# Optimization experiments

Measured on AMD Instinct MI355X. Metric: run time of the kernel, lower is better.

The kernel has to match this reference:

```python
import jax, jax.numpy as jnp
import numpy as np

N = 50000          # total nodes
B = 10             # graphs in batch
NPG = N // B       # nodes per graph (equal-sized graphs)
E = 800000         # edges
IN_DIM = 128
HID = 128
NHEAD = 4
DHEAD = HID // NHEAD
T = 1000
SLOPE = 0.2        # leaky_relu negative slope
ALPHA_L = 2.0


def _ln(x, g=None, b=None, eps=1e-5):
    mu = jnp.mean(x, axis=-1, keepdims=True)
    var = jnp.var(x, axis=-1, keepdims=True)
    y = (x - mu) * jax.lax.rsqrt(var + eps)
    if g is not None:
        y = y * g + b
    return y


def _gatv2(h, src, dst, Ws, Wd, a, b):
    # DGL GATv2Conv, share_weights=False, residual=False, bias=True, activation=gelu
    fs = (h @ Ws).reshape(N, NHEAD, DHEAD)
    fd = (h @ Wd).reshape(N, NHEAD, DHEAD)
    # per-edge attention logits [E, NHEAD]
    e = jnp.sum(jax.nn.leaky_relu(fs[src] + fd[dst], SLOPE) * a, axis=-1)
    # edge softmax grouped by destination node
    m = jax.ops.segment_max(e, dst, num_segments=N)
    ee = jnp.exp(e - m[dst])
    den = jax.ops.segment_sum(ee, dst, num_segments=N)
    alpha = ee / den[dst]                                  # [E, NHEAD]
    rst = jax.ops.segment_sum(alpha[..., None] * fs[src], dst, num_segments=N)
    rst = jax.nn.gelu(rst + b.reshape(1, NHEAD, DHEAD), approximate=False)
    return rst.reshape(N, HID)


def _forward(x, noise, sab, somab, time_emb,
             Ws0, Wd0, a0, b0, g0, be0,
             Ws1, Wd1, a1, b1, g1, be1,
             Wo1, bo1, Wo2, bo2, src, dst, t):
    # sample_q: statistics-matched signed noise
    miu = jnp.mean(x, axis=0)
    std = jnp.std(x, axis=0, ddof=1)          # torch.std is unbiased
    nz = _ln(noise) * std + miu
    nz = jnp.sign(x) * jnp.abs(nz)
    s1 = jnp.repeat(sab[t], NPG)[:, None]
    s2 = jnp.repeat(somab[t], NPG)[:, None]
    x_t = s1 * x + s2 * nz
    temb = jnp.repeat(time_emb[t], NPG, axis=0)
    # Denoising_Unet
    h = jnp.concatenate([x_t, temb], axis=1)   # [N, IN_DIM+HID]
    h = _ln(_gatv2(h, src, dst, Ws0, Wd0, a0, b0), g0, be0)
    h_in = h
    h = _gatv2(h, src, dst, Ws1, Wd1, a1, b1)
    h = _ln(h + h_in, g1, be1)                 # residual (shapes match)
    out = jax.nn.relu(h @ Wo1 + bo1) @ Wo2 + bo2
    # loss_fn
    mse = jnp.mean((out - x) ** 2)
    on = out / jnp.maximum(jnp.linalg.norm(out, axis=-1, keepdims=True), 1e-12)
    xn = x / jnp.maximum(jnp.linalg.norm(x, axis=-1, keepdims=True), 1e-12)
    cos = jnp.mean((1.0 - jnp.sum(on * xn, axis=-1)) ** ALPHA_L)
    return mse + 0.1 * cos


def setup_inputs() -> dict:
    key = jax.random.key(0)
    ks = jax.random.split(key, 26)
    betas = np.linspace(1e-4, 0.02, T, dtype=np.float64)
    ab = np.cumprod(1.0 - betas)
    s = 0.02
    in0 = IN_DIM + HID
    inp = {}
    inp['x'] = jax.random.normal(ks[0], (N, IN_DIM), jnp.float32)
    inp['noise'] = jax.random.normal(ks[1], (N, IN_DIM), jnp.float32)
    inp['src'] = jax.random.randint(ks[2], (E,), 0, N, dtype=jnp.int32)
    inp['dst'] = jax.random.randint(ks[3], (E,), 0, N, dtype=jnp.int32)
    inp['t'] = jax.random.randint(ks[4], (B,), 0, T, dtype=jnp.int32)
    inp['sab'] = jnp.asarray(np.sqrt(ab), jnp.float32)
    inp['somab'] = jnp.asarray(np.sqrt(1.0 - ab), jnp.float32)
    inp['time_emb'] = jax.random.normal(ks[5], (T, HID), jnp.float32) * s
    inp['Ws0'] = jax.random.normal(ks[6], (in0, HID), jnp.float32) * s
    inp['Wd0'] = jax.random.normal(ks[7], (in0, HID), jnp.float32) * s
    inp['a0'] = jax.random.normal(ks[8], (NHEAD, DHEAD), jnp.float32) * s
    inp['b0'] = jnp.zeros((HID,), jnp.float32)
    inp['g0'] = jnp.ones((HID,), jnp.float32)
    inp['be0'] = jnp.zeros((HID,), jnp.float32)
    inp['Ws1'] = jax.random.normal(ks[9], (HID, HID), jnp.float32) * s
    inp['Wd1'] = jax.random.normal(ks[10], (HID, HID), jnp.float32) * s
    inp['a1'] = jax.random.normal(ks[11], (NHEAD, DHEAD), jnp.float32) * s
    inp['b1'] = jnp.zeros((HID,), jnp.float32)
    inp['g1'] = jnp.ones((HID,), jnp.float32)
    inp['be1'] = jnp.zeros((HID,), jnp.float32)
    inp['Wo1'] = jax.random.normal(ks[12], (HID, HID), jnp.float32) * s
    inp['bo1'] = jnp.zeros((HID,), jnp.float32)
    inp['Wo2'] = jax.random.normal(ks[13], (HID, IN_DIM), jnp.float32) * s
    inp['bo2'] = jnp.zeros((IN_DIM,), jnp.float32)
    return inp


def reference(x, noise, src, dst, t, sab, somab, time_emb,
              Ws0, Wd0, a0, b0, g0, be0,
              Ws1, Wd1, a1, b1, g1, be1,
              Wo1, bo1, Wo2, bo2):
    return _forward(x, noise, sab, somab, time_emb,
                    Ws0, Wd0, a0, b0, g0, be0,
                    Ws1, Wd1, a1, b1, g1, be1,
                    Wo1, bo1, Wo2, bo2, src, dst, t)
```

## Files before the change

kernel.cpp:

```cpp
#include <hip/hip_runtime.h>
#include <hip/hip_bf16.h>
#include <math.h>

#define NN 50000
#define EE 800000
#define NPG 5000

typedef short bf16x8 __attribute__((ext_vector_type(8)));
typedef float f32x4 __attribute__((ext_vector_type(4)));

__device__ __forceinline__ float gelu_exact(float v) {
    return 0.5f * v * (1.0f + erff(v * 0.70710678118654752440f));
}

__device__ __forceinline__ ushort f2b(float f) {
    union { float f; uint u; } v; v.f = f;
    uint r = (v.u + 0x7fffu + ((v.u >> 16) & 1)) >> 16;
    return (ushort)r;
}
__device__ __forceinline__ uint pack2(float a, float b) {
    return (uint)f2b(a) | ((uint)f2b(b) << 16);
}
__device__ __forceinline__ float blo(uint u) {
    union { uint u; float f; } v; v.u = u << 16; return v.f;
}
__device__ __forceinline__ float bhi(uint u) {
    union { uint u; float f; } v; v.u = u & 0xffff0000u; return v.f;
}

__global__ __launch_bounds__(256) void head1_kernel(const float* __restrict__ x,
        float* __restrict__ sums, const int* __restrict__ dst, int* __restrict__ counts,
        const float* __restrict__ Ws0, const float* __restrict__ Wd0,
        const float* __restrict__ Ws1, const float* __restrict__ Wd1,
        const float* __restrict__ Wo1, const float* __restrict__ Wo2,
        ushort* __restrict__ Wt0, ushort* __restrict__ Wt1,
        ushort* __restrict__ Wo1t, ushort* __restrict__ Wo2t) {
    int bid = blockIdx.x;
    int tid = threadIdx.x;
    if (bid < 1024) {
        int col4 = (tid & 31) * 4;
        int rowgrp = tid >> 5;
        float s0 = 0.f, s1 = 0.f, s2 = 0.f, s3 = 0.f;
        float q0 = 0.f, q1 = 0.f, q2 = 0.f, q3 = 0.f;
        for (int r = bid * 8 + rowgrp; r < NN; r += 8192) {
            float4 v = *(const float4*)(x + (size_t)r * 128 + col4);
            s0 += v.x; s1 += v.y; s2 += v.z; s3 += v.w;
            q0 += v.x * v.x; q1 += v.y * v.y; q2 += v.z * v.z; q3 += v.w * v.w;
        }
        s0 += __shfl_xor(s0, 32); s1 += __shfl_xor(s1, 32);
        s2 += __shfl_xor(s2, 32); s3 += __shfl_xor(s3, 32);
        q0 += __shfl_xor(q0, 32); q1 += __shfl_xor(q1, 32);
        q2 += __shfl_xor(q2, 32); q3 += __shfl_xor(q3, 32);
        __shared__ float red[4][32][8];
        int wv = tid >> 6, l = tid & 63;
        if (l < 32) {
            float* p = red[wv][l];
            p[0] = s0; p[1] = s1; p[2] = s2; p[3] = s3;
            p[4] = q0; p[5] = q1; p[6] = q2; p[7] = q3;
        }
        __syncthreads();
        if (tid < 32) {
            float a0 = 0.f, a1 = 0.f, a2 = 0.f, a3 = 0.f;
            float b0 = 0.f, b1 = 0.f, b2 = 0.f, b3 = 0.f;
#pragma unroll
            for (int w = 0; w < 4; ++w) {
                float* p = red[w][tid];
                a0 += p[0]; a1 += p[1]; a2 += p[2]; a3 += p[3];
                b0 += p[4]; b1 += p[5]; b2 += p[6]; b3 += p[7];
            }
            int c = tid * 4;
            atomicAdd(&sums[c], a0); atomicAdd(&sums[c + 1], a1);
            atomicAdd(&sums[c + 2], a2); atomicAdd(&sums[c + 3], a3);
            atomicAdd(&sums[128 + c], b0); atomicAdd(&sums[128 + c + 1], b1);
            atomicAdd(&sums[128 + c + 2], b2); atomicAdd(&sums[128 + c + 3], b3);
        }
    } else if (bid < 4149) {
        int i = (bid - 1024) * 256 + tid;
        if (i < EE) atomicAdd(&counts[dst[i]], 1);
    } else {
        int i = (bid - 4149) * 256 + tid;
        if (i < 65536) {
            int c = i >> 8, k = i & 255;
            const float* W = (c < 128) ? Ws0 : Wd0;
            Wt0[c * 256 + k] = f2b(W[k * 128 + (c & 127)]);
        } else if (i < 98304) {
            int j = i - 65536;
            int c = j >> 7, k = j & 127;
            const float* W = (c < 128) ? Ws1 : Wd1;
            Wt1[c * 128 + k] = f2b(W[k * 128 + (c & 127)]);
        } else if (i < 114688) {
            int j = i - 98304;
            int c = j >> 7, k = j & 127;
            Wo1t[c * 128 + k] = f2b(Wo1[k * 128 + c]);
        } else if (i < 131072) {
            int j = i - 114688;
            int c = j >> 7, k = j & 127;
            Wo2t[c * 128 + k] = f2b(Wo2[k * 128 + c]);
        }
    }
}

__global__ __launch_bounds__(1024) void head2_kernel(const int* __restrict__ counts,
        int* __restrict__ blockSums, float* __restrict__ stats, int n) {
    int bid = blockIdx.x;
    int tid = threadIdx.x;
    if (bid < 49) {
        int i = bid * 1024 + tid;
        int v = (i < n) ? counts[i] : 0;
#pragma unroll
        for (int o = 32; o > 0; o >>= 1) v += __shfl_down(v, o);
        __shared__ int sh[16];
        int lane = tid & 63, wv = tid >> 6;
        if (lane == 0) sh[wv] = v;
        __syncthreads();
        if (tid == 0) {
            int s = 0;
#pragma unroll
            for (int k = 0; k < 16; ++k) s += sh[k];
            blockSums[bid] = s;
        }
    } else {
        if (tid < 128) {
            int c = tid;
            float sum = stats[c], sumsq = stats[128 + c];
            float mu = sum / (float)n;
            float var = (sumsq - sum * sum / (float)n) / (float)(n - 1);
            stats[256 + c] = mu;
            stats[384 + c] = sqrtf(fmaxf(var, 0.f));
        }
    }
}

__global__ __launch_bounds__(1024) void head3_kernel(const float* __restrict__ x,
        const float* __restrict__ noise, const int* __restrict__ t,
        const float* __restrict__ sab, const float* __restrict__ somab,
        const float* __restrict__ temb, const float* __restrict__ stats,
        ushort* __restrict__ h,
        const int* __restrict__ counts, const int* __restrict__ blockSums,
        int* __restrict__ indptr, int* __restrict__ cursor, int n) {
    int bid = blockIdx.x;
    int tid = threadIdx.x;
    if (bid < 3125) {
        int wid = bid * 16 + (tid >> 6);
        int lane = tid & 63;
        int tt = t[wid / NPG];
        float s1 = sab[tt], s2v = somab[tt];
        float2 nz = ((const float2*)noise)[(size_t)wid * 64 + lane];
        float s = nz.x + nz.y;
        float sq = nz.x * nz.x + nz.y * nz.y;
#pragma unroll
        for (int o = 1; o < 64; o <<= 1) { s += __shfl_xor(s, o); sq += __shfl_xor(sq, o); }
        float mu = s * (1.f / 128.f);
        float var = sq * (1.f / 128.f) - mu * mu;
        float r = rsqrtf(var + 1e-5f);
        int f0 = 2 * lane, f1 = f0 + 1;
        float y0 = (nz.x - mu) * r * stats[384 + f0] + stats[256 + f0];
        float y1 = (nz.y - mu) * r * stats[384 + f1] + stats[256 + f1];
        float2 xv = ((const float2*)x)[(size_t)wid * 64 + lane];
        float sg0 = (xv.x > 0.f) ? 1.f : ((xv.x < 0.f) ? -1.f : 0.f);
        float sg1 = (xv.y > 0.f) ? 1.f : ((xv.y < 0.f) ? -1.f : 0.f);
        float n0 = sg0 * fabsf(y0);
        float n1 = sg1 * fabsf(y1);
        float xt0 = s1 * xv.x + s2v * n0;
        float xt1 = s1 * xv.y + s2v * n1;
        uint* row = (uint*)(h + (size_t)wid * 256);
        row[lane] = pack2(xt0, xt1);
        float2 te = ((const float2*)(temb + (size_t)tt * 128))[lane];
        row[64 + lane] = pack2(te.x, te.y);
    } else {
        int b = bid - 3125;
        __shared__ int sOff, sTot;
        if (tid < 64) {
            int v = (tid < 49) ? blockSums[tid] : 0;
            int incl = v;
#pragma unroll
            for (int o = 1; o < 64; o <<= 1) {
                int tv = __shfl_up(incl, o);
                if ((tid & 63) >= o) incl += tv;
            }
            int off = (b == 0) ? 0 : __shfl(incl, b - 1);
            int tot = __shfl(incl, 48);
            if (tid == 0) { sOff = off; sTot = tot; }
        }
        __syncthreads();
        int i = b * 1024 + tid;
        int v = (i < n) ? counts[i] : 0;
        int lane = tid & 63, wv = tid >> 6;
        int incl = v;
#pragma unroll
        for (int o = 1; o < 64; o <<= 1) {
            int tv = __shfl_up(incl, o);
            if (lane >= o) incl += tv;
        }
        __shared__ int wsum[16];
        __shared__ int woff[16];
        if (lane == 63) wsum[wv] = incl;
        __syncthreads();
        if (tid == 0) {
            int s = 0;
#pragma unroll
            for (int k = 0; k < 16; ++k) { woff[k] = s; s += wsum[k]; }
        }
        __syncthreads();
        int ex = incl - v + woff[wv] + sOff;
        if (i < n) { indptr[i] = ex; cursor[i] = ex; }
        if (b == 48 && tid == 0) indptr[n] = sTot;
    }
}

__global__ __launch_bounds__(1024) void scatter_kernel(const int* __restrict__ src,
        const int* __restrict__ dst, int* __restrict__ cursor,
        int* __restrict__ csr_src, int e) {
    int i = blockIdx.x * 1024 + threadIdx.x;
    if (i < e) {
        int p = atomicAdd(&cursor[dst[i]], 1);
        csr_src[p] = src[i];
    }
}

template<int K, int NCOL, int EPI>
__global__ __launch_bounds__(256, 2) void mfma_gemm(const ushort* __restrict__ A,
        const ushort* __restrict__ Wt, const float* __restrict__ bias,
        ushort* __restrict__ C0, ushort* __restrict__ C1,
        float* __restrict__ Cf, int M) {
    constexpr int NFRAG = NCOL / 16;
    constexpr int KSTEPS = K / 32;
    __shared__ ushort Bs[32 * NCOL];
    int tid = threadIdx.x;
    int wave = tid >> 6, lane = tid & 63;
    int l15 = lane & 15, g = lane >> 4;
    int rowBase = blockIdx.x * 64 + wave * 16;
    int r = rowBase + l15;
    int rc = min(r, M - 1);
    const ushort* Arow = A + (size_t)rc * K + g * 8;

    f32x4 acc[NFRAG] = {};

    for (int ks = 0; ks < KSTEPS; ++ks) {
#pragma unroll
        for (int i = 0; i < NCOL / 64; ++i) {
            int ch = tid + i * 256;
            int c = ch >> 2, q = ch & 3;
            float4 v = *(const float4*)(Wt + (size_t)c * K + ks * 32 + q * 8);
            int off = c * 64 + ((q * 16) ^ ((c & 7) << 4));
            *(float4*)((char*)Bs + off) = v;
        }
        __syncthreads();
        bf16x8 af = *(const bf16x8*)(Arow + ks * 32);
        int roff = l15 * 64 + ((g * 16) ^ ((l15 & 7) << 4));
#pragma unroll
        for (int n = 0; n < NFRAG; ++n) {
            bf16x8 bf = *(const bf16x8*)((const char*)Bs + n * 1024 + roff);
            acc[n] = __builtin_amdgcn_mfma_f32_16x16x32_bf16(af, bf, acc[n], 0, 0, 0);
        }
        __syncthreads();
    }

#pragma unroll
    for (int n = 0; n < NFRAG; ++n) {
        int col = n * 16 + l15;
#pragma unroll
        for (int j = 0; j < 4; ++j) {
            int row = rowBase + g * 4 + j;
            if (row < M) {
                float v = acc[n][j];
                if (EPI == 1) v = fmaxf(v + bias[col], 0.f);
                if (EPI == 2) v = v + bias[col];
                if (EPI == 2) {
                    Cf[(size_t)row * 128 + col] = v;
                } else {
                    ushort bv = f2b(v);
                    if (NCOL == 256) {
                        if (n < 8) C0[(size_t)row * 128 + col] = bv;
                        else       C1[(size_t)row * 128 + col - 128] = bv;
                    } else {
                        C0[(size_t)row * 128 + col] = bv;
                    }
                }
            }
        }
    }
}

__global__ __launch_bounds__(256) void gat_ln_kernel(const ushort* __restrict__ fs,
        const ushort* __restrict__ fd, const float* __restrict__ a,
        const float* __restrict__ bias, const int* __restrict__ indptr,
        const int* __restrict__ csr_src, const float* __restrict__ resid,
        const float* __restrict__ g, const float* __restrict__ be,
        float* __restrict__ outF, ushort* __restrict__ outB, int n) {
    int wid = (blockIdx.x * blockDim.x + threadIdx.x) >> 6;
    int lane = threadIdx.x & 63;
    if (wid >= n) return;
    int beg = indptr[wid], cnt = indptr[wid + 1] - beg;
    const int* ip = csr_src + beg;
    uint fdu = ((const uint*)fd)[(size_t)wid * 64 + lane];
    float fd0 = blo(fdu), fd1 = bhi(fdu);
    float a0 = a[2 * lane], a1 = a[2 * lane + 1];
    const uint* fsu = (const uint*)fs;

    int e0 = (0 < cnt) ? ip[0] : 0;
    int e1 = (1 < cnt) ? ip[1] : 0;
    int e2 = (2 < cnt) ? ip[2] : 0;
    int e3 = (3 < cnt) ? ip[3] : 0;
    int e4 = (4 < cnt) ? ip[4] : 0;
    int e5 = (5 < cnt) ? ip[5] : 0;
    int e6 = (6 < cnt) ? ip[6] : 0;
    int e7 = (7 < cnt) ? ip[7] : 0;
    uint v0 = fsu[(size_t)e0 * 64 + lane];
    uint v1 = fsu[(size_t)e1 * 64 + lane];
    uint v2 = fsu[(size_t)e2 * 64 + lane];
    uint v3 = fsu[(size_t)e3 * 64 + lane];
    uint v4 = fsu[(size_t)e4 * 64 + lane];
    uint v5 = fsu[(size_t)e5 * 64 + lane];
    uint v6 = fsu[(size_t)e6 * 64 + lane];
    uint v7 = fsu[(size_t)e7 * 64 + lane];

    float den = 0.f, acc0 = 0.f, acc1 = 0.f;
    for (int j = 0; j < cnt; ++j) {
        uint cur = v0;
        v0 = v1; v1 = v2; v2 = v3; v3 = v4; v4 = v5; v5 = v6; v6 = v7;
        int nj = j + 8;
        int ni = (nj < cnt) ? ip[nj] : 0;
        v7 = fsu[(size_t)ni * 64 + lane];
        float c0f = blo(cur), c1f = bhi(cur);
        float t0 = c0f + fd0; t0 = (t0 > 0.f ? t0 : 0.2f * t0) * a0;
        float t1 = c1f + fd1; t1 = (t1 > 0.f ? t1 : 0.2f * t1) * a1;
        float p = t0 + t1;
        p += __shfl_xor(p, 1); p += __shfl_xor(p, 2);
        p += __shfl_xor(p, 4); p += __shfl_xor(p, 8);
        float w = __expf(p);
        den += w;
        acc0 = fmaf(w, c0f, acc0);
        acc1 = fmaf(w, c1f, acc1);
    }

    float inv = (cnt > 0) ? 1.f / den : 0.f;
    float r0 = gelu_exact(acc0 * inv + bias[2 * lane]);
    float r1 = gelu_exact(acc1 * inv + bias[2 * lane + 1]);
    if (resid) {
        float2 rr = ((const float2*)resid)[(size_t)wid * 64 + lane];
        r0 += rr.x; r1 += rr.y;
    }
    float s = r0 + r1;
    float sq = r0 * r0 + r1 * r1;
#pragma unroll
    for (int o = 1; o < 64; o <<= 1) { s += __shfl_xor(s, o); sq += __shfl_xor(sq, o); }
    float mu = s * (1.f / 128.f);
    float var = sq * (1.f / 128.f) - mu * mu;
    float rstd = rsqrtf(var + 1e-5f);
    float2 gg = ((const float2*)g)[lane];
    float2 bb = ((const float2*)be)[lane];
    float o0 = (r0 - mu) * rstd * gg.x + bb.x;
    float o1 = (r1 - mu) * rstd * gg.y + bb.y;
    if (outF) ((float2*)outF)[(size_t)wid * 64 + lane] = make_float2(o0, o1);
    if (outB) ((uint*)outB)[(size_t)wid * 64 + lane] = pack2(o0, o1);
}

__global__ __launch_bounds__(256) void loss_partial_kernel(const float* __restrict__ out,
        const float* __restrict__ x, float* __restrict__ partials, int n) {
    __shared__ float sm[8];
    int lane = threadIdx.x & 63;
    int wv = threadIdx.x >> 6;
    int gw = blockIdx.x * 4 + wv;
    float d2 = 0.f, closs = 0.f;
    for (int row = gw; row < n; row += 4096) {
        float2 o = ((const float2*)out)[(size_t)row * 64 + lane];
        float2 xv = ((const float2*)x)[(size_t)row * 64 + lane];
        float e0 = o.x - xv.x, e1 = o.y - xv.y;
        d2 += e0 * e0 + e1 * e1;
        float oo = o.x * o.x + o.y * o.y;
        float xx = xv.x * xv.x + xv.y * xv.y;
        float ox = o.x * xv.x + o.y * xv.y;
#pragma unroll
        for (int s = 1; s < 64; s <<= 1) {
            oo += __shfl_xor(oo, s); xx += __shfl_xor(xx, s); ox += __shfl_xor(ox, s);
        }
        float no = fmaxf(sqrtf(oo), 1e-12f);
        float nx = fmaxf(sqrtf(xx), 1e-12f);
        float cs = 1.f - ox / (no * nx);
        closs += cs * cs;
    }
#pragma unroll
    for (int s = 1; s < 64; s <<= 1) d2 += __shfl_xor(d2, s);
    if (lane == 0) { sm[wv] = d2; sm[4 + wv] = closs; }
    __syncthreads();
    if (threadIdx.x == 0) {
        partials[2 * blockIdx.x] = sm[0] + sm[1] + sm[2] + sm[3];
        partials[2 * blockIdx.x + 1] = sm[4] + sm[5] + sm[6] + sm[7];
    }
}

__global__ __launch_bounds__(1024) void loss_final_kernel(const float* __restrict__ partials,
        float* __restrict__ outp, int nb, int n) {
    __shared__ double sd[32];
    int tid = threadIdx.x;
    double m = 0.0, c = 0.0;
    for (int i = tid; i < nb; i += 1024) { m += partials[2 * i]; c += partials[2 * i + 1]; }
#pragma unroll
    for (int s = 1; s < 64; s <<= 1) { m += __shfl_xor(m, s); c += __shfl_xor(c, s); }
    int wv = tid >> 6, lane = tid & 63;
    if (lane == 0) { sd[wv] = m; sd[16 + wv] = c; }
    __syncthreads();
    if (tid == 0) {
        double mt = 0.0, ct = 0.0;
        for (int i = 0; i < 16; ++i) { mt += sd[i]; ct += sd[16 + i]; }
        outp[0] = (float)(mt / ((double)n * 128.0) + 0.1 * ct / (double)n);
    }
}

extern "C" void kernel_launch(void* const* d_in, const int* in_sizes, int n_in,
                              void* d_out, int out_size, void* d_ws, size_t ws_size,
                              hipStream_t stream) {
    const int N = NN, E = EE;
    const float* x     = (const float*)d_in[0];
    const float* noise = (const float*)d_in[1];
    const int*   src   = (const int*)d_in[2];
    const int*   dst   = (const int*)d_in[3];
    const int*   t     = (const int*)d_in[4];
    const float* sab   = (const float*)d_in[5];
    const float* somab = (const float*)d_in[6];
    const float* temb  = (const float*)d_in[7];
    const float* Ws0   = (const float*)d_in[8];
    const float* Wd0   = (const float*)d_in[9];
    const float* a0    = (const float*)d_in[10];
    const float* b0    = (const float*)d_in[11];
    const float* g0    = (const float*)d_in[12];
    const float* be0   = (const float*)d_in[13];
    const float* Ws1   = (const float*)d_in[14];
    const float* Wd1   = (const float*)d_in[15];
    const float* a1    = (const float*)d_in[16];
    const float* b1    = (const float*)d_in[17];
    const float* g1    = (const float*)d_in[18];
    const float* be1   = (const float*)d_in[19];
    const float* Wo1   = (const float*)d_in[20];
    const float* bo1   = (const float*)d_in[21];
    const float* Wo2   = (const float*)d_in[22];
    const float* bo2   = (const float*)d_in[23];

    float* ws = (float*)d_ws;
    ushort* hB  = (ushort*)ws;
    ushort* Pb  = (ushort*)ws;
    ushort* fsB = (ushort*)(ws + (size_t)N * 128);
    ushort* fdB = (ushort*)(ws + (size_t)N * 192);
    float*  P   = ws + (size_t)N * 256;
    float*  outb = P;
    ushort* Qb  = fdB;
    ushort* z   = fsB;
    float* wtail = ws + (size_t)N * 384;
    ushort* Wt0  = (ushort*)wtail;
    ushort* Wt1  = (ushort*)(wtail + 32768);
    ushort* Wo1t = (ushort*)(wtail + 49152);
    ushort* Wo2t = (ushort*)(wtail + 57344);
    float* stats    = wtail + 65536;
    float* partials = stats + 512;
    int* counts  = (int*)(partials + 2048);
    int* indptr  = counts + N;
    int* cursor  = indptr + N + 1;
    int* csr_src = cursor + N;
    int* blockSums = csr_src + E;

    hipMemsetAsync(stats, 0, 512 * sizeof(float), stream);
    hipMemsetAsync(counts, 0, (size_t)N * sizeof(int), stream);

    head1_kernel<<<4661, 256, 0, stream>>>(x, stats, dst, counts,
                                           Ws0, Wd0, Ws1, Wd1, Wo1, Wo2,
                                           Wt0, Wt1, Wo1t, Wo2t);
    head2_kernel<<<50, 1024, 0, stream>>>(counts, blockSums, stats, N);
    head3_kernel<<<3174, 1024, 0, stream>>>(x, noise, t, sab, somab, temb, stats, hB,
                                            counts, blockSums, indptr, cursor, N);
    scatter_kernel<<<(E + 1023) / 1024, 1024, 0, stream>>>(src, dst, cursor, csr_src, E);

    int gemmGrid = (N + 63) / 64;
    mfma_gemm<256, 256, 0><<<gemmGrid, 256, 0, stream>>>(hB, Wt0, nullptr, fsB, fdB, nullptr, N);
    gat_ln_kernel<<<(N + 3) / 4, 256, 0, stream>>>(fsB, fdB, a0, b0, indptr, csr_src,
                                                   nullptr, g0, be0, P, Pb, N);
    mfma_gemm<128, 256, 0><<<gemmGrid, 256, 0, stream>>>(Pb, Wt1, nullptr, fsB, fdB, nullptr, N);
    gat_ln_kernel<<<(N + 3) / 4, 256, 0, stream>>>(fsB, fdB, a1, b1, indptr, csr_src,
                                                   P, g1, be1, nullptr, Qb, N);
    mfma_gemm<128, 128, 1><<<gemmGrid, 256, 0, stream>>>(Qb, Wo1t, bo1, z, nullptr, nullptr, N);
    mfma_gemm<128, 128, 2><<<gemmGrid, 256, 0, stream>>>(z, Wo2t, bo2, nullptr, nullptr, outb, N);

    loss_partial_kernel<<<1024, 256, 0, stream>>>(outb, x, partials, N);
    loss_final_kernel<<<1, 1024, 0, stream>>>(partials, (float*)d_out, 1024, N);
}
```

Measured before the change: 454.8 us.

## Fuse loss into final GEMM epilogue and vectorize GAT aggregation per quad

The final output GEMM now computes the MSE and cosine loss terms in its epilogue and accumulates them with atomics. This removes the fp32 output buffer write, the separate loss_partial pass and the multi-block final reduction. The GAT kernel now handles four edges at once, one per 16-lane quad, with each lane loading 16 bytes (8 bf16), which cuts serial loop iterations and shuffle depth. The layer-1 residual is also read from the bf16 copy instead of a separate fp32 copy, which drops that fp32 write and trades some precision and ordering determinism of the float atomics for lower memory traffic.

```diff
diff --git a/kernel.cpp b/kernel.cpp
--- a/kernel.cpp
+++ b/kernel.cpp
@@ -26,6 +26,10 @@
 }
 __device__ __forceinline__ float bhi(uint u) {
     union { uint u; float f; } v; v.u = u & 0xffff0000u; return v.f;
+}
+__device__ __forceinline__ void unpack8(uint4 u, float* f) {
+    f[0] = blo(u.x); f[1] = bhi(u.x); f[2] = blo(u.y); f[3] = bhi(u.y);
+    f[4] = blo(u.z); f[5] = bhi(u.z); f[6] = blo(u.w); f[7] = bhi(u.w);
 }
 
 __global__ __launch_bounds__(256) void head1_kernel(const float* __restrict__ x,
@@ -222,7 +226,7 @@
 __global__ __launch_bounds__(256, 2) void mfma_gemm(const ushort* __restrict__ A,
         const ushort* __restrict__ Wt, const float* __restrict__ bias,
         ushort* __restrict__ C0, ushort* __restrict__ C1,
-        float* __restrict__ Cf, int M) {
+        const float* __restrict__ X, float* __restrict__ lossAcc, int M) {
     constexpr int NFRAG = NCOL / 16;
     constexpr int KSTEPS = K / 32;
     __shared__ ushort Bs[32 * NCOL];
@@ -256,19 +260,16 @@
         __syncthreads();
     }
 
-#pragma unroll
-    for (int n = 0; n < NFRAG; ++n) {
-        int col = n * 16 + l15;
-#pragma unroll
-        for (int j = 0; j < 4; ++j) {
-            int row = rowBase + g * 4 + j;
-            if (row < M) {
-                float v = acc[n][j];
-                if (EPI == 1) v = fmaxf(v + bias[col], 0.f);
-                if (EPI == 2) v = v + bias[col];
-                if (EPI == 2) {
-                    Cf[(size_t)row * 128 + col] = v;
-                } else {
+    if (EPI != 3) {
+#pragma unroll
+        for (int n = 0; n < NFRAG; ++n) {
+            int col = n * 16 + l15;
+#pragma unroll
+            for (int j = 0; j < 4; ++j) {
+                int row = rowBase + g * 4 + j;
+                if (row < M) {
+                    float v = acc[n][j];
+                    if (EPI == 1) v = fmaxf(v + bias[col], 0.f);
                     ushort bv = f2b(v);
                     if (NCOL == 256) {
                         if (n < 8) C0[(size_t)row * 128 + col] = bv;
@@ -279,133 +280,161 @@
                 }
             }
         }
+    } else {
+        float td2 = 0.f, tcl = 0.f;
+#pragma unroll
+        for (int j = 0; j < 4; ++j) {
+            int row = rowBase + g * 4 + j;
+            bool rv = row < M;
+            float d2 = 0.f, oo = 0.f, xx = 0.f, ox = 0.f;
+#pragma unroll
+            for (int n = 0; n < NFRAG; ++n) {
+                int col = n * 16 + l15;
+                float o = rv ? (acc[n][j] + bias[col]) : 0.f;
+                float xv = rv ? X[(size_t)row * 128 + col] : 0.f;
+                float e = o - xv;
+                d2 += e * e; oo += o * o; xx += xv * xv; ox += o * xv;
+            }
+#pragma unroll
+            for (int off = 1; off < 16; off <<= 1) {
+                d2 += __shfl_xor(d2, off); oo += __shfl_xor(oo, off);
+                xx += __shfl_xor(xx, off); ox += __shfl_xor(ox, off);
+            }
+            if (rv) {
+                float no = fmaxf(sqrtf(oo), 1e-12f);
+                float nx = fmaxf(sqrtf(xx), 1e-12f);
+                float cs = 1.f - ox / (no * nx);
+                td2 += d2; tcl += cs * cs;
+            }
+        }
+        __shared__ float sd2[16], scl[16];
+        if (l15 == 0) { sd2[wave * 4 + g] = td2; scl[wave * 4 + g] = tcl; }
+        __syncthreads();
+        if (tid == 0) {
+            float a2 = 0.f, ac = 0.f;
+#pragma unroll
+            for (int k2 = 0; k2 < 16; ++k2) { a2 += sd2[k2]; ac += scl[k2]; }
+            atomicAdd(&lossAcc[0], a2);
+            atomicAdd(&lossAcc[1], ac);
+        }
     }
 }
 
 __global__ __launch_bounds__(256) void gat_ln_kernel(const ushort* __restrict__ fs,
         const ushort* __restrict__ fd, const float* __restrict__ a,
         const float* __restrict__ bias, const int* __restrict__ indptr,
-        const int* __restrict__ csr_src, const float* __restrict__ resid,
+        const int* __restrict__ csr_src, const ushort* __restrict__ residB,
         const float* __restrict__ g, const float* __restrict__ be,
-        float* __restrict__ outF, ushort* __restrict__ outB, int n) {
+        ushort* __restrict__ outB, int n) {
     int wid = (blockIdx.x * blockDim.x + threadIdx.x) >> 6;
     int lane = threadIdx.x & 63;
     if (wid >= n) return;
+    int quad = lane >> 4, s = lane & 15;
     int beg = indptr[wid], cnt = indptr[wid + 1] - beg;
     const int* ip = csr_src + beg;
-    uint fdu = ((const uint*)fd)[(size_t)wid * 64 + lane];
-    float fd0 = blo(fdu), fd1 = bhi(fdu);
-    float a0 = a[2 * lane], a1 = a[2 * lane + 1];
-    const uint* fsu = (const uint*)fs;
-
-    int e0 = (0 < cnt) ? ip[0] : 0;
-    int e1 = (1 < cnt) ? ip[1] : 0;
-    int e2 = (2 < cnt) ? ip[2] : 0;
-    int e3 = (3 < cnt) ? ip[3] : 0;
-    int e4 = (4 < cnt) ? ip[4] : 0;
-    int e5 = (5 < cnt) ? ip[5] : 0;
-    int e6 = (6 < cnt) ? ip[6] : 0;
-    int e7 = (7 < cnt) ? ip[7] : 0;
-    uint v0 = fsu[(size_t)e0 * 64 + lane];
-    uint v1 = fsu[(size_t)e1 * 64 + lane];
-    uint v2 = fsu[(size_t)e2 * 64 + lane];
-    uint v3 = fsu[(size_t)e3 * 64 + lane];
-    uint v4 = fsu[(size_t)e4 * 64 + lane];
-    uint v5 = fsu[(size_t)e5 * 64 + lane];
-    uint v6 = fsu[(size_t)e6 * 64 + lane];
-    uint v7 = fsu[(size_t)e7 * 64 + lane];
-
-    float den = 0.f, acc0 = 0.f, acc1 = 0.f;
-    for (int j = 0; j < cnt; ++j) {
-        uint cur = v0;
-        v0 = v1; v1 = v2; v2 = v3; v3 = v4; v4 = v5; v5 = v6; v6 = v7;
-        int nj = j + 8;
-        int ni = (nj < cnt) ? ip[nj] : 0;
-        v7 = fsu[(size_t)ni * 64 + lane];
-        float c0f = blo(cur), c1f = bhi(cur);
-        float t0 = c0f + fd0; t0 = (t0 > 0.f ? t0 : 0.2f * t0) * a0;
-        float t1 = c1f + fd1; t1 = (t1 > 0.f ? t1 : 0.2f * t1) * a1;
-        float p = t0 + t1;
-        p += __shfl_xor(p, 1); p += __shfl_xor(p, 2);
-        p += __shfl_xor(p, 4); p += __shfl_xor(p, 8);
-        float w = __expf(p);
+    const uint4* fs4 = (const uint4*)fs;
+
+    uint4 fdq = ((const uint4*)fd)[(size_t)wid * 16 + s];
+    float fdv[8]; unpack8(fdq, fdv);
+    float av[8];
+    {
+        float4 a0 = *(const float4*)(a + 8 * s);
+        float4 a1 = *(const float4*)(a + 8 * s + 4);
+        av[0] = a0.x; av[1] = a0.y; av[2] = a0.z; av[3] = a0.w;
+        av[4] = a1.x; av[5] = a1.y; av[6] = a1.z; av[7] = a1.w;
+    }
+
+    int i0 = (quad < cnt) ? ip[quad] : 0;
+    int i1 = (4 + quad < cnt) ? ip[4 + quad] : 0;
+    uint4 vA = fs4[(size_t)i0 * 16 + s];
+    uint4 vB = fs4[(size_t)i1 * 16 + s];
+    int p0 = (8  < cnt) ? ip[8]  : 0;
+    int p1 = (9  < cnt) ? ip[9]  : 0;
+    int p2 = (10 < cnt) ? ip[10] : 0;
+    int p3 = (11 < cnt) ? ip[11] : 0;
+
+    float den = 0.f;
+    float acc[8] = {};
+    for (int j = 0; j < cnt; j += 4) {
+        uint4 cur = vA; vA = vB;
+        int pe = (quad == 0) ? p0 : (quad == 1) ? p1 : (quad == 2) ? p2 : p3;
+        vB = fs4[(size_t)pe * 16 + s];
+        p0 = (j + 12 < cnt) ? ip[j + 12] : 0;
+        p1 = (j + 13 < cnt) ? ip[j + 13] : 0;
+        p2 = (j + 14 < cnt) ? ip[j + 14] : 0;
+        p3 = (j + 15 < cnt) ? ip[j + 15] : 0;
+        float c[8]; unpack8(cur, c);
+        float p = 0.f;
+#pragma unroll
+        for (int i = 0; i < 8; ++i) {
+            float tv = c[i] + fdv[i];
+            tv = (tv > 0.f) ? tv : 0.2f * tv;
+            p = fmaf(tv, av[i], p);
+        }
+        p += __shfl_xor(p, 1);
+        p += __shfl_xor(p, 2);
+        float w = (j + quad < cnt) ? __expf(p) : 0.f;
         den += w;
-        acc0 = fmaf(w, c0f, acc0);
-        acc1 = fmaf(w, c1f, acc1);
-    }
-
+#pragma unroll
+        for (int i = 0; i < 8; ++i) acc[i] = fmaf(w, c[i], acc[i]);
+    }
+#pragma unroll
+    for (int i = 0; i < 8; ++i) {
+        acc[i] += __shfl_xor(acc[i], 16);
+        acc[i] += __shfl_xor(acc[i], 32);
+    }
+    den += __shfl_xor(den, 16);
+    den += __shfl_xor(den, 32);
     float inv = (cnt > 0) ? 1.f / den : 0.f;
-    float r0 = gelu_exact(acc0 * inv + bias[2 * lane]);
-    float r1 = gelu_exact(acc1 * inv + bias[2 * lane + 1]);
-    if (resid) {
-        float2 rr = ((const float2*)resid)[(size_t)wid * 64 + lane];
-        r0 += rr.x; r1 += rr.y;
-    }
-    float s = r0 + r1;
-    float sq = r0 * r0 + r1 * r1;
-#pragma unroll
-    for (int o = 1; o < 64; o <<= 1) { s += __shfl_xor(s, o); sq += __shfl_xor(sq, o); }
-    float mu = s * (1.f / 128.f);
-    float var = sq * (1.f / 128.f) - mu * mu;
+
+    float bi[8];
+    {
+        float4 b0v = *(const float4*)(bias + 8 * s);
+        float4 b1v = *(const float4*)(bias + 8 * s + 4);
+        bi[0] = b0v.x; bi[1] = b0v.y; bi[2] = b0v.z; bi[3] = b0v.w;
+        bi[4] = b1v.x; bi[5] = b1v.y; bi[6] = b1v.z; bi[7] = b1v.w;
+    }
+    float r[8];
+#pragma unroll
+    for (int i = 0; i < 8; ++i) r[i] = gelu_exact(acc[i] * inv + bi[i]);
+    if (residB) {
+        uint4 rq = ((const uint4*)residB)[(size_t)wid * 16 + s];
+        float rv[8]; unpack8(rq, rv);
+#pragma unroll
+        for (int i = 0; i < 8; ++i) r[i] += rv[i];
+    }
+    float ssum = 0.f, ssq = 0.f;
+#pragma unroll
+    for (int i = 0; i < 8; ++i) { ssum += r[i]; ssq += r[i] * r[i]; }
+#pragma unroll
+    for (int o = 1; o < 16; o <<= 1) { ssum += __shfl_xor(ssum, o); ssq += __shfl_xor(ssq, o); }
+    float mu = ssum * (1.f / 128.f);
+    float var = ssq * (1.f / 128.f) - mu * mu;
     float rstd = rsqrtf(var + 1e-5f);
-    float2 gg = ((const float2*)g)[lane];
-    float2 bb = ((const float2*)be)[lane];
-    float o0 = (r0 - mu) * rstd * gg.x + bb.x;
-    float o1 = (r1 - mu) * rstd * gg.y + bb.y;
-    if (outF) ((float2*)outF)[(size_t)wid * 64 + lane] = make_float2(o0, o1);
-    if (outB) ((uint*)outB)[(size_t)wid * 64 + lane] = pack2(o0, o1);
-}
-
-__global__ __launch_bounds__(256) void loss_partial_kernel(const float* __restrict__ out,
-        const float* __restrict__ x, float* __restrict__ partials, int n) {
-    __shared__ float sm[8];
-    int lane = threadIdx.x & 63;
-    int wv = threadIdx.x >> 6;
-    int gw = blockIdx.x * 4 + wv;
-    float d2 = 0.f, closs = 0.f;
-    for (int row = gw; row < n; row += 4096) {
-        float2 o = ((const float2*)out)[(size_t)row * 64 + lane];
-        float2 xv = ((const float2*)x)[(size_t)row * 64 + lane];
-        float e0 = o.x - xv.x, e1 = o.y - xv.y;
-        d2 += e0 * e0 + e1 * e1;
-        float oo = o.x * o.x + o.y * o.y;
-        float xx = xv.x * xv.x + xv.y * xv.y;
-        float ox = o.x * xv.x + o.y * xv.y;
-#pragma unroll
-        for (int s = 1; s < 64; s <<= 1) {
-            oo += __shfl_xor(oo, s); xx += __shfl_xor(xx, s); ox += __shfl_xor(ox, s);
-        }
-        float no = fmaxf(sqrtf(oo), 1e-12f);
-        float nx = fmaxf(sqrtf(xx), 1e-12f);
-        float cs = 1.f - ox / (no * nx);
-        closs += cs * cs;
-    }
-#pragma unroll
-    for (int s = 1; s < 64; s <<= 1) d2 += __shfl_xor(d2, s);
-    if (lane == 0) { sm[wv] = d2; sm[4 + wv] = closs; }
-    __syncthreads();
-    if (threadIdx.x == 0) {
-        partials[2 * blockIdx.x] = sm[0] + sm[1] + sm[2] + sm[3];
-        partials[2 * blockIdx.x + 1] = sm[4] + sm[5] + sm[6] + sm[7];
-    }
-}
-
-__global__ __launch_bounds__(1024) void loss_final_kernel(const float* __restrict__ partials,
-        float* __restrict__ outp, int nb, int n) {
-    __shared__ double sd[32];
-    int tid = threadIdx.x;
-    double m = 0.0, c = 0.0;
-    for (int i = tid; i < nb; i += 1024) { m += partials[2 * i]; c += partials[2 * i + 1]; }
-#pragma unroll
-    for (int s = 1; s < 64; s <<= 1) { m += __shfl_xor(m, s); c += __shfl_xor(c, s); }
-    int wv = tid >> 6, lane = tid & 63;
-    if (lane == 0) { sd[wv] = m; sd[16 + wv] = c; }
-    __syncthreads();
-    if (tid == 0) {
-        double mt = 0.0, ct = 0.0;
-        for (int i = 0; i < 16; ++i) { mt += sd[i]; ct += sd[16 + i]; }
-        outp[0] = (float)(mt / ((double)n * 128.0) + 0.1 * ct / (double)n);
-    }
+    float gv[8], bv[8];
+    {
+        float4 g0v = *(const float4*)(g + 8 * s);
+        float4 g1v = *(const float4*)(g + 8 * s + 4);
+        gv[0] = g0v.x; gv[1] = g0v.y; gv[2] = g0v.z; gv[3] = g0v.w;
+        gv[4] = g1v.x; gv[5] = g1v.y; gv[6] = g1v.z; gv[7] = g1v.w;
+        float4 e0v = *(const float4*)(be + 8 * s);
+        float4 e1v = *(const float4*)(be + 8 * s + 4);
+        bv[0] = e0v.x; bv[1] = e0v.y; bv[2] = e0v.z; bv[3] = e0v.w;
+        bv[4] = e1v.x; bv[5] = e1v.y; bv[6] = e1v.z; bv[7] = e1v.w;
+    }
+    float o_[8];
+#pragma unroll
+    for (int i = 0; i < 8; ++i) o_[i] = (r[i] - mu) * rstd * gv[i] + bv[i];
+    if (quad == 0) {
+        uint4 w4;
+        w4.x = pack2(o_[0], o_[1]); w4.y = pack2(o_[2], o_[3]);
+        w4.z = pack2(o_[4], o_[5]); w4.w = pack2(o_[6], o_[7]);
+        ((uint4*)outB)[(size_t)wid * 16 + s] = w4;
+    }
+}
+
+__global__ void loss_final2(const float* __restrict__ lossAcc, float* __restrict__ outp, int n) {
+    outp[0] = lossAcc[0] / ((float)n * 128.f) + 0.1f * (lossAcc[1] / (float)n);
 }
 
 extern "C" void kernel_launch(void* const* d_in, const int* in_sizes, int n_in,
@@ -442,8 +471,6 @@
     ushort* Pb  = (ushort*)ws;
     ushort* fsB = (ushort*)(ws + (size_t)N * 128);
     ushort* fdB = (ushort*)(ws + (size_t)N * 192);
-    float*  P   = ws + (size_t)N * 256;
-    float*  outb = P;
     ushort* Qb  = fdB;
     ushort* z   = fsB;
     float* wtail = ws + (size_t)N * 384;
@@ -452,14 +479,14 @@
     ushort* Wo1t = (ushort*)(wtail + 49152);
     ushort* Wo2t = (ushort*)(wtail + 57344);
     float* stats    = wtail + 65536;
-    float* partials = stats + 512;
-    int* counts  = (int*)(partials + 2048);
+    float* lossAcc  = stats + 512;
+    int* counts  = (int*)(lossAcc + 2048);
     int* indptr  = counts + N;
     int* cursor  = indptr + N + 1;
     int* csr_src = cursor + N;
     int* blockSums = csr_src + E;
 
-    hipMemsetAsync(stats, 0, 512 * sizeof(float), stream);
+    hipMemsetAsync(stats, 0, 514 * sizeof(float), stream);
     hipMemsetAsync(counts, 0, (size_t)N * sizeof(int), stream);
 
     head1_kernel<<<4661, 256, 0, stream>>>(x, stats, dst, counts,
@@ -471,15 +498,17 @@
     scatter_kernel<<<(E + 1023) / 1024, 1024, 0, stream>>>(src, dst, cursor, csr_src, E);
 
     int gemmGrid = (N + 63) / 64;
-    mfma_gemm<256, 256, 0><<<gemmGrid, 256, 0, stream>>>(hB, Wt0, nullptr, fsB, fdB, nullptr, N);
+    mfma_gemm<256, 256, 0><<<gemmGrid, 256, 0, stream>>>(hB, Wt0, nullptr, fsB, fdB,
+                                                         nullptr, nullptr, N);
     gat_ln_kernel<<<(N + 3) / 4, 256, 0, stream>>>(fsB, fdB, a0, b0, indptr, csr_src,
-                                                   nullptr, g0, be0, P, Pb, N);
-    mfma_gemm<128, 256, 0><<<gemmGrid, 256, 0, stream>>>(Pb, Wt1, nullptr, fsB, fdB, nullptr, N);
+                                                   nullptr, g0, be0, Pb, N);
+    mfma_gemm<128, 256, 0><<<gemmGrid, 256, 0, stream>>>(Pb, Wt1, nullptr, fsB, fdB,
+                                                         nullptr, nullptr, N);
     gat_ln_kernel<<<(N + 3) / 4, 256, 0, stream>>>(fsB, fdB, a1, b1, indptr, csr_src,
-                                                   P, g1, be1, nullptr, Qb, N);
-    mfma_gemm<128, 128, 1><<<gemmGrid, 256, 0, stream>>>(Qb, Wo1t, bo1, z, nullptr, nullptr, N);
-    mfma_gemm<128, 128, 2><<<gemmGrid, 256, 0, stream>>>(z, Wo2t, bo2, nullptr, nullptr, outb, N);
-
-    loss_partial_kernel<<<1024, 256, 0, stream>>>(outb, x, partials, N);
-    loss_final_kernel<<<1, 1024, 0, stream>>>(partials, (float*)d_out, 1024, N);
-}
+                                                   Pb, g1, be1, Qb, N);
+    mfma_gemm<128, 128, 1><<<gemmGrid, 256, 0, stream>>>(Qb, Wo1t, bo1, z, nullptr,
+                                                         nullptr, nullptr, N);
+    mfma_gemm<128, 128, 3><<<gemmGrid, 256, 0, stream>>>(z, Wo2t, bo2, nullptr, nullptr,
+                                                         x, lossAcc, N);
+    loss_final2<<<1, 1, 0, stream>>>(lossAcc, (float*)d_out, N);
+}
```

Result: faster. 400.7 us (-11.9%).
